# Kernel optimization log

Hardware: AMD Instinct MI355X
Metric: run time of the kernel (lower is better)

The kernel has to match this reference:

```python
import jax, jax.numpy as jnp
import numpy as np

NUM_EMBEDDINGS = 1024
EMBEDDING_DIM = 64
COMMITMENT_COST = 0.1
DECAY = 0.9
EPSILON = 1e-05


def setup_inputs() -> dict:
    key = jax.random.key(0)
    k1, k2, k3 = jax.random.split(key, 3)
    inputs = jax.random.normal(k1, (16, EMBEDDING_DIM, 4096), dtype=jnp.float32)
    embedding_weight = jax.random.normal(k2, (NUM_EMBEDDINGS, EMBEDDING_DIM), dtype=jnp.float32)
    ema_cluster_size = jnp.zeros((NUM_EMBEDDINGS,), dtype=jnp.float32)
    ema_w = jax.random.normal(k3, (NUM_EMBEDDINGS, EMBEDDING_DIM), dtype=jnp.float32)
    return {
        "inputs": inputs,
        "embedding_weight": embedding_weight,
        "ema_cluster_size": ema_cluster_size,
        "ema_w": ema_w,
    }


def reference(inputs, embedding_weight, ema_cluster_size, ema_w):
    K, D = embedding_weight.shape
    # (B, C, L) -> (B, L, C); C == embedding_dim
    x = jnp.transpose(inputs, (0, 2, 1))
    B, L, _ = x.shape
    flat = x.reshape(-1, D)  # [N, D], N = B*L
    N = flat.shape[0]

    distances = (
        jnp.sum(flat * flat, axis=1, keepdims=True)
        + jnp.sum(embedding_weight * embedding_weight, axis=1)
        - 2.0 * (flat @ embedding_weight.T)
    )
    idx = jnp.argmin(distances, axis=1)  # [N] int

    # embedding lookup (equivalent to one-hot @ weight)
    quantized = embedding_weight[idx].reshape(B, L, D)

    # one-hot column sums and scatter-reduction, without materializing [N, K]
    counts = jnp.zeros((K,), dtype=flat.dtype).at[idx].add(1.0)  # sum(encodings, 0)
    dw = jax.ops.segment_sum(flat, idx, num_segments=K)  # encodings^T @ flat_input

    # EMA updates (training path)
    cs = ema_cluster_size * DECAY + (1.0 - DECAY) * counts
    n = jnp.sum(cs)
    cs = (cs + EPSILON) / (n + K * EPSILON) * n
    new_ema_w = ema_w * DECAY + (1.0 - DECAY) * dw
    new_embedding_weight = new_ema_w / cs[:, None]

    # KLDivLoss(batchmean)(softmax(quantized.detach()), softmax(inputs)) over dim=2
    p_in = jax.nn.softmax(jax.lax.stop_gradient(quantized), axis=2)
    p_tgt = jax.nn.softmax(x, axis=2)
    kl = jnp.sum(p_tgt * (jnp.log(p_tgt) - p_in)) / B
    loss = COMMITMENT_COST * kl

    # straight-through estimator
    quantized_st = x + jax.lax.stop_gradient(quantized - x)

    avg_probs = counts / N
    perplexity = jnp.exp(-jnp.sum(avg_probs * jnp.log(avg_probs + 1e-10)))

    out = jnp.transpose(quantized_st, (0, 2, 1))  # back to (B, C, L)
    encoding_indices = idx[:, None]
    return (out, loss, perplexity, new_embedding_weight, encoding_indices)
```

## Files before the change

### kernel.cpp

```cpp
#include <hip/hip_runtime.h>

#define LDIM 4096
#define DDIM 64
#define KCODES 1024
#define BDIM 16
#define NROWS 65536
#define NSLICE 8
#define SLICE_ROWS (NROWS / NSLICE)

typedef __attribute__((ext_vector_type(8))) short short8;
typedef __attribute__((ext_vector_type(16))) float float16v;

__device__ __forceinline__ unsigned int orderf(float f) {
  unsigned int u = __float_as_uint(f);
  return (u & 0x80000000u) ? ~u : (u | 0x80000000u);
}

__device__ __forceinline__ unsigned long long shfl_xor_u64(unsigned long long v, int m) {
  int lo = __shfl_xor((int)(unsigned int)(v & 0xffffffffull), m, 64);
  int hi = __shfl_xor((int)(unsigned int)(v >> 32), m, 64);
  return ((unsigned long long)(unsigned int)hi << 32) | (unsigned int)lo;
}

__device__ __forceinline__ unsigned int bf16_rne(float x) {
  unsigned int u = __float_as_uint(x);
  return (u + 0x7FFFu + ((u >> 16) & 1u)) >> 16;
}

__global__ void prep_kernel(const float* __restrict__ Ew,
                            float* __restrict__ enorm,
                            float* __restrict__ SE,
                            unsigned short* __restrict__ Epk2) {
  int k = blockIdx.x;
  int d = threadIdx.x;
  float v = Ew[k * DDIM + d];
  float n2 = v * v;
  #pragma unroll
  for (int o = 32; o > 0; o >>= 1) n2 += __shfl_xor(n2, o, 64);
  float m = v;
  #pragma unroll
  for (int o = 32; o > 0; o >>= 1) m = fmaxf(m, __shfl_xor(m, o, 64));
  float e = __expf(v - m);
  float Z = e;
  #pragma unroll
  for (int o = 32; o > 0; o >>= 1) Z += __shfl_xor(Z, o, 64);
  SE[k * DDIM + d] = e / Z;
  if (d == 0) enorm[k] = n2;

  unsigned int rh = bf16_rne(v);
  float hif = __uint_as_float(rh << 16);
  unsigned int rl = bf16_rne(v - hif);
  int tile = k >> 5, mm = k & 31;
  int s = d >> 4, h = (d >> 3) & 1, j = d & 7;
  int base = tile * 4096 + (h * 32 + mm) * 8 + j;
  Epk2[base + s * 512]        = (unsigned short)rh;
  Epk2[base + (4 + s) * 512]  = (unsigned short)rl;
}

__launch_bounds__(256, 2)
__global__ void argmin_kernel(const float* __restrict__ inp,
                              const unsigned short* __restrict__ Epk2,
                              const float* __restrict__ enorm,
                              int* __restrict__ idx_ws,
                              float* __restrict__ outidx) {
  const int tid = threadIdx.x;
  const int lane = tid & 63;
  const int w = tid >> 6;
  const int half = lane >> 5;
  const int m = lane & 31;
  const int row_base = blockIdx.x * 128 + w * 32;
  const int b = row_base >> 12;
  const int l0 = row_base & 4095;
  const float* xp = inp + (size_t)b * DDIM * LDIM + l0 + m;

  short8 afr[8];
  #pragma unroll
  for (int s = 0; s < 4; s++) {
    #pragma unroll
    for (int j = 0; j < 8; j++) {
      int d = 16 * s + 8 * half + j;
      float x = xp[(size_t)d * LDIM];
      unsigned int rh = bf16_rne(x);
      float hif = __uint_as_float(rh << 16);
      unsigned int rl = bf16_rne(x - hif);
      afr[s][j] = (short)(unsigned short)rh;
      afr[4 + s][j] = (short)(unsigned short)rl;
    }
  }

  float bsc[16];
  int bix[16];
  #pragma unroll
  for (int j = 0; j < 16; j++) { bsc[j] = 1e30f; bix[j] = 0; }

  const unsigned short* eb = Epk2 + lane * 8;

  short8 bA[8], bB[8];
  float enA, enB;

  #pragma unroll
  for (int s = 0; s < 4; s++) {
    bA[s]     = *(const short8*)(eb + s * 512);
    bA[4 + s] = *(const short8*)(eb + 2048 + s * 512);
  }
  enA = enorm[m];

  #pragma unroll 1
  for (int i = 0; i < 16; i++) {
    const int tB = 2 * i + 1;
    {
      const unsigned short* p = eb + tB * 4096;
      #pragma unroll
      for (int s = 0; s < 4; s++) {
        bB[s]     = *(const short8*)(p + s * 512);
        bB[4 + s] = *(const short8*)(p + 2048 + s * 512);
      }
      enB = enorm[tB * 32 + m];
    }
    {
      float16v a0 = {}, a1 = {}, a2 = {};
      #pragma unroll
      for (int s = 0; s < 4; s++) {
        a0 = __builtin_amdgcn_mfma_f32_32x32x16_bf16(afr[s], bA[s], a0, 0, 0, 0);
        a1 = __builtin_amdgcn_mfma_f32_32x32x16_bf16(afr[s], bA[4 + s], a1, 0, 0, 0);
        a2 = __builtin_amdgcn_mfma_f32_32x32x16_bf16(afr[4 + s], bA[s], a2, 0, 0, 0);
      }
      int ci = 2 * i * 32 + m;
      #pragma unroll
      for (int j = 0; j < 16; j++) {
        float sc = fmaf(-2.f, a0[j] + a1[j] + a2[j], enA);
        if (sc < bsc[j]) { bsc[j] = sc; bix[j] = ci; }
      }
    }
    if (i < 15) {
      const unsigned short* p = eb + (2 * i + 2) * 4096;
      #pragma unroll
      for (int s = 0; s < 4; s++) {
        bA[s]     = *(const short8*)(p + s * 512);
        bA[4 + s] = *(const short8*)(p + 2048 + s * 512);
      }
      enA = enorm[(2 * i + 2) * 32 + m];
    }
    {
      float16v a0 = {}, a1 = {}, a2 = {};
      #pragma unroll
      for (int s = 0; s < 4; s++) {
        a0 = __builtin_amdgcn_mfma_f32_32x32x16_bf16(afr[s], bB[s], a0, 0, 0, 0);
        a1 = __builtin_amdgcn_mfma_f32_32x32x16_bf16(afr[s], bB[4 + s], a1, 0, 0, 0);
        a2 = __builtin_amdgcn_mfma_f32_32x32x16_bf16(afr[4 + s], bB[s], a2, 0, 0, 0);
      }
      int ci = tB * 32 + m;
      #pragma unroll
      for (int j = 0; j < 16; j++) {
        float sc = fmaf(-2.f, a0[j] + a1[j] + a2[j], enB);
        if (sc < bsc[j]) { bsc[j] = sc; bix[j] = ci; }
      }
    }
  }

  #pragma unroll
  for (int j = 0; j < 16; j++) {
    unsigned long long key =
        ((unsigned long long)orderf(bsc[j]) << 32) | (unsigned int)bix[j];
    #pragma unroll
    for (int mm = 1; mm < 32; mm <<= 1) {
      unsigned long long o = shfl_xor_u64(key, mm);
      if (o < key) key = o;
    }
    if (m == 0) {
      int row_local = (j & 3) + 8 * (j >> 2) + 4 * half;
      int grow = row_base + row_local;
      int cidx = (int)(key & 0xffffffffull);
      idx_ws[grow] = cidx;
      outidx[grow] = (float)cidx;
    }
  }
}

__launch_bounds__(256)
__global__ void outkl_dw_kernel(const float* __restrict__ inp,
                                const float* __restrict__ Ew,
                                const float* __restrict__ SE,
                                const int* __restrict__ idx_ws,
                                float* __restrict__ out,
                                float* __restrict__ klacc,
                                float* __restrict__ partial,
                                float* __restrict__ pcounts) {
  __shared__ float lds[2 * KCODES];
  const int tid = threadIdx.x;

  if (blockIdx.x < 1024) {
    float* Zs  = lds;
    float* S1s = lds + 256;
    float* Us  = lds + 512;
    const int c = tid >> 6;
    const int i = tid & 63;
    const int r = blockIdx.x * 64 + i;
    const int b = r >> 12, l = r & 4095;
    const float* xp = inp + (size_t)b * DDIM * LDIM + l;
    float* op = out + (size_t)b * DDIM * LDIM + l;
    const int k = idx_ws[r];
    const float4* Ek4 = (const float4*)(Ew + k * DDIM) + c * 4;
    const float4* Qk4 = (const float4*)(SE + k * DDIM) + c * 4;

    float Z = 0.f, S1 = 0.f, U = 0.f;
    #pragma unroll
    for (int t = 0; t < 4; t++) {
      float ek[4], qk[4];
      *(float4*)ek = Ek4[t];
      *(float4*)qk = Qk4[t];
      #pragma unroll
      for (int u = 0; u < 4; u++) {
        int d = c * 16 + t * 4 + u;
        float x = xp[(size_t)d * LDIM];
        float e = __expf(x);
        Z += e;
        S1 += e * x;
        U += e * qk[u];
        op[(size_t)d * LDIM] = ek[u];
      }
    }
    Zs[c * 64 + i] = Z; S1s[c * 64 + i] = S1; Us[c * 64 + i] = U;
    __syncthreads();
    if (tid < 64) {
      float Zt = Zs[i] + Zs[64 + i] + Zs[128 + i] + Zs[192 + i];
      float S1t = S1s[i] + S1s[64 + i] + S1s[128 + i] + S1s[192 + i];
      float Ut = Us[i] + Us[64 + i] + Us[128 + i] + Us[192 + i];
      float kl = (S1t - Ut) / Zt - __logf(Zt);
      #pragma unroll
      for (int o = 32; o > 0; o >>= 1) kl += __shfl_xor(kl, o, 64);
      if (i == 0) atomicAdd(klacc, kl);
    }
  } else {
    float* dwp = lds;
    float* cnt = lds + KCODES;
    const int bid = blockIdx.x - 1024;
    const int d = bid & 63;
    const int slice = bid >> 6;
    const bool do_cnt = (d == 0);

    #pragma unroll
    for (int i = 0; i < KCODES / 256; i++) {
      dwp[tid + i * 256] = 0.f;
      cnt[tid + i * 256] = 0.f;
    }
    __syncthreads();

    const int r0 = slice * SLICE_ROWS;
    for (int i = tid; i < SLICE_ROWS; i += 256) {
      int r = r0 + i;
      int b = r >> 12, l = r & 4095;
      float x = inp[(size_t)b * DDIM * LDIM + (size_t)d * LDIM + l];
      int k = idx_ws[r];
      atomicAdd(&dwp[k], x);
      if (do_cnt) atomicAdd(&cnt[k], 1.0f);
    }
    __syncthreads();

    float* dst = partial + ((size_t)slice * 64 + d) * KCODES;
    #pragma unroll
    for (int i = 0; i < KCODES / 256; i++) dst[tid + i * 256] = dwp[tid + i * 256];
    if (do_cnt) {
      float* cd = pcounts + (size_t)slice * KCODES;
      #pragma unroll
      for (int i = 0; i < KCODES / 256; i++) cd[tid + i * 256] = cnt[tid + i * 256];
    }
  }
}

__launch_bounds__(256)
__global__ void finalize_kernel(const float* __restrict__ partial,
                                const float* __restrict__ pcounts,
                                const float* __restrict__ emaw,
                                const float* __restrict__ emacs,
                                const float* __restrict__ klacc,
                                float* __restrict__ emb_out,
                                float* __restrict__ loss_out,
                                float* __restrict__ perp_out) {
  __shared__ float red[4], red2[4];
  const int tid = threadIdx.x;
  const int i = blockIdx.x * 256 + tid;
  const int k = i >> 6, d = i & 63;

  float se = 0.f;
  #pragma unroll
  for (int t = 0; t < 4; t++) se += emacs[tid * 4 + t];
  #pragma unroll
  for (int o = 32; o > 0; o >>= 1) se += __shfl_xor(se, o, 64);
  if ((tid & 63) == 0) red[tid >> 6] = se;
  __syncthreads();
  const float S = red[0] + red[1] + red[2] + red[3];
  const float N = 0.9f * S + 0.1f * (float)NROWS;

  float c = 0.f;
  #pragma unroll
  for (int sl = 0; sl < NSLICE; sl++) c += pcounts[sl * KCODES + k];
  float cs = fmaf(0.1f, c, emacs[k] * 0.9f);
  float csp = (cs + 1e-5f) / (N + (float)KCODES * 1e-5f) * N;

  float s = 0.f;
  #pragma unroll
  for (int sl = 0; sl < NSLICE; sl++)
    s += partial[((size_t)sl * 64 + d) * KCODES + k];
  emb_out[i] = fmaf(0.1f, s, emaw[i] * 0.9f) / csp;

  if (blockIdx.x == 0) {
    float es = 0.f;
    #pragma unroll
    for (int t = 0; t < 4; t++) {
      int kk = tid * 4 + t;
      float cc = 0.f;
      #pragma unroll
      for (int sl = 0; sl < NSLICE; sl++) cc += pcounts[sl * KCODES + kk];
      float a = cc * (1.0f / (float)NROWS);
      es += a * logf(a + 1e-10f);
    }
    #pragma unroll
    for (int o = 32; o > 0; o >>= 1) es += __shfl_xor(es, o, 64);
    if ((tid & 63) == 0) red2[tid >> 6] = es;
    __syncthreads();
    if (tid == 0) {
      *perp_out = expf(-(red2[0] + red2[1] + red2[2] + red2[3]));
      *loss_out = 0.1f * (*klacc) * (1.0f / 16.0f);
    }
  }
}

extern "C" void kernel_launch(void* const* d_in, const int* in_sizes, int n_in,
                              void* d_out, int out_size, void* d_ws, size_t ws_size,
                              hipStream_t stream) {
  const float* inp   = (const float*)d_in[0];
  const float* Ew    = (const float*)d_in[1];
  const float* emacs = (const float*)d_in[2];
  const float* emaw  = (const float*)d_in[3];

  float* out      = (float*)d_out;
  float* loss_out = out + 4194304;
  float* perp_out = out + 4194305;
  float* emb_out  = out + 4194306;
  float* idxf_out = out + 4194306 + 65536;

  char* ws = (char*)d_ws;
  int*   idx_ws  = (int*)(ws);
  float* klacc   = (float*)(ws + 262144);
  float* enorm   = (float*)(ws + 266496);
  float* SE      = (float*)(ws + 274688);
  unsigned short* Epk2 = (unsigned short*)(ws + 536832);
  float* partial = (float*)(ws + 536832);
  float* pcounts = (float*)(ws + 2633984);

  hipMemsetAsync(ws + 262144, 0, 256, stream);

  prep_kernel<<<KCODES, 64, 0, stream>>>(Ew, enorm, SE, Epk2);
  argmin_kernel<<<512, 256, 0, stream>>>(inp, Epk2, enorm, idx_ws, idxf_out);
  outkl_dw_kernel<<<1536, 256, 0, stream>>>(inp, Ew, SE, idx_ws, out, klacc,
                                            partial, pcounts);
  finalize_kernel<<<NROWS / 256, 256, 0, stream>>>(partial, pcounts, emaw, emacs,
                                                   klacc, emb_out, loss_out,
                                                   perp_out);
}
```

Before: 164.1 us.

## Restage codeword gather through LDS for vectorized output writes and KL

The output/KL branch now handles 256 rows per block instead of 64. Each block gathers the selected codewords and softmax rows into LDS in transposed form, so input reads and output writes become float4 accesses along L rather than scalar strided accesses. Block order is swapped so the scatter-reduction (dw) blocks launch first, and the grid shrinks from 1536 to 768 blocks. The cost is about 46KB of LDS per block, which reduces occupancy, plus extra __syncthreads per 16-dim chunk.

```diff
diff --git a/kernel.cpp b/kernel.cpp
--- a/kernel.cpp
+++ b/kernel.cpp
@@ -186,57 +186,14 @@
                                 float* __restrict__ klacc,
                                 float* __restrict__ partial,
                                 float* __restrict__ pcounts) {
-  __shared__ float lds[2 * KCODES];
+  __shared__ float smem[11528];
   const int tid = threadIdx.x;
 
-  if (blockIdx.x < 1024) {
-    float* Zs  = lds;
-    float* S1s = lds + 256;
-    float* Us  = lds + 512;
-    const int c = tid >> 6;
-    const int i = tid & 63;
-    const int r = blockIdx.x * 64 + i;
-    const int b = r >> 12, l = r & 4095;
-    const float* xp = inp + (size_t)b * DDIM * LDIM + l;
-    float* op = out + (size_t)b * DDIM * LDIM + l;
-    const int k = idx_ws[r];
-    const float4* Ek4 = (const float4*)(Ew + k * DDIM) + c * 4;
-    const float4* Qk4 = (const float4*)(SE + k * DDIM) + c * 4;
-
-    float Z = 0.f, S1 = 0.f, U = 0.f;
-    #pragma unroll
-    for (int t = 0; t < 4; t++) {
-      float ek[4], qk[4];
-      *(float4*)ek = Ek4[t];
-      *(float4*)qk = Qk4[t];
-      #pragma unroll
-      for (int u = 0; u < 4; u++) {
-        int d = c * 16 + t * 4 + u;
-        float x = xp[(size_t)d * LDIM];
-        float e = __expf(x);
-        Z += e;
-        S1 += e * x;
-        U += e * qk[u];
-        op[(size_t)d * LDIM] = ek[u];
-      }
-    }
-    Zs[c * 64 + i] = Z; S1s[c * 64 + i] = S1; Us[c * 64 + i] = U;
-    __syncthreads();
-    if (tid < 64) {
-      float Zt = Zs[i] + Zs[64 + i] + Zs[128 + i] + Zs[192 + i];
-      float S1t = S1s[i] + S1s[64 + i] + S1s[128 + i] + S1s[192 + i];
-      float Ut = Us[i] + Us[64 + i] + Us[128 + i] + Us[192 + i];
-      float kl = (S1t - Ut) / Zt - __logf(Zt);
-      #pragma unroll
-      for (int o = 32; o > 0; o >>= 1) kl += __shfl_xor(kl, o, 64);
-      if (i == 0) atomicAdd(klacc, kl);
-    }
-  } else {
-    float* dwp = lds;
-    float* cnt = lds + KCODES;
-    const int bid = blockIdx.x - 1024;
-    const int d = bid & 63;
-    const int slice = bid >> 6;
+  if (blockIdx.x < 512) {
+    float* dwp = smem;
+    float* cnt = smem + KCODES;
+    const int d = blockIdx.x & 63;
+    const int slice = blockIdx.x >> 6;
     const bool do_cnt = (d == 0);
 
     #pragma unroll
@@ -265,6 +222,91 @@
       #pragma unroll
       for (int i = 0; i < KCODES / 256; i++) cd[tid + i * 256] = cnt[tid + i * 256];
     }
+  } else {
+    int*   kk  = (int*)smem;
+    float* Et  = smem + 256;
+    float* Qt  = smem + 4352;
+    float* Zp  = smem + 8448;
+    float* S1p = smem + 9472;
+    float* Up  = smem + 10496;
+    float* red4 = smem + 11520;
+
+    const int obid = blockIdx.x - 512;
+    const int r0 = obid * 256;
+    const int b = r0 >> 12;
+    const int l0 = r0 & 4095;
+    const float* xbase = inp + (size_t)b * DDIM * LDIM + l0;
+    float* obase = out + (size_t)b * DDIM * LDIM + l0;
+    const int w = tid >> 6, lane = tid & 63;
+
+    kk[tid] = idx_ws[r0 + tid];
+    __syncthreads();
+    const int myk = kk[tid];
+    const int gi = ((tid & 3) << 6) | (tid >> 2);
+
+    float Zc[4] = {0.f, 0.f, 0.f, 0.f};
+    float S1c[4] = {0.f, 0.f, 0.f, 0.f};
+    float Uc[4] = {0.f, 0.f, 0.f, 0.f};
+
+    #pragma unroll 1
+    for (int c = 0; c < 4; c++) {
+      {
+        const float4* Ep = (const float4*)(Ew + myk * DDIM + c * 16);
+        const float4* Qp = (const float4*)(SE + myk * DDIM + c * 16);
+        #pragma unroll
+        for (int q = 0; q < 4; q++) {
+          float4 ev = Ep[q], qv = Qp[q];
+          Et[(4 * q + 0) * 256 + tid] = ev.x;
+          Et[(4 * q + 1) * 256 + tid] = ev.y;
+          Et[(4 * q + 2) * 256 + tid] = ev.z;
+          Et[(4 * q + 3) * 256 + tid] = ev.w;
+          Qt[(4 * q + 0) * 256 + gi] = qv.x;
+          Qt[(4 * q + 1) * 256 + gi] = qv.y;
+          Qt[(4 * q + 2) * 256 + gi] = qv.z;
+          Qt[(4 * q + 3) * 256 + gi] = qv.w;
+        }
+      }
+      __syncthreads();
+      #pragma unroll
+      for (int t = 0; t < 4; t++) {
+        const int dq = 4 * w + t;
+        const int d = c * 16 + dq;
+        float4 xv = *(const float4*)(xbase + (size_t)d * LDIM + lane * 4);
+        float4 ov = *(const float4*)&Et[dq * 256 + lane * 4];
+        *(float4*)(obase + (size_t)d * LDIM + lane * 4) = ov;
+        #pragma unroll
+        for (int j = 0; j < 4; j++) {
+          float x = (j == 0) ? xv.x : (j == 1) ? xv.y : (j == 2) ? xv.z : xv.w;
+          float e = __expf(x);
+          Zc[j] += e;
+          S1c[j] += e * x;
+          Uc[j] += e * Qt[dq * 256 + (j << 6) + lane];
+        }
+      }
+      __syncthreads();
+    }
+
+    #pragma unroll
+    for (int j = 0; j < 4; j++) {
+      Zp[w * 256 + 4 * lane + j] = Zc[j];
+      S1p[w * 256 + 4 * lane + j] = S1c[j];
+      Up[w * 256 + 4 * lane + j] = Uc[j];
+    }
+    __syncthreads();
+    float Z = 0.f, S1 = 0.f, U = 0.f;
+    #pragma unroll
+    for (int w2 = 0; w2 < 4; w2++) {
+      Z += Zp[w2 * 256 + tid];
+      S1 += S1p[w2 * 256 + tid];
+      U += Up[w2 * 256 + tid];
+    }
+    float kl = (S1 - U) / Z - __logf(Z);
+    #pragma unroll
+    for (int o = 32; o > 0; o >>= 1) kl += __shfl_xor(kl, o, 64);
+    if (lane == 0) red4[w] = kl;
+    __syncthreads();
+    if (tid == 0)
+      atomicAdd(klacc, red4[0] + red4[1] + red4[2] + red4[3]);
   }
 }
 
@@ -353,8 +395,8 @@
 
   prep_kernel<<<KCODES, 64, 0, stream>>>(Ew, enorm, SE, Epk2);
   argmin_kernel<<<512, 256, 0, stream>>>(inp, Epk2, enorm, idx_ws, idxf_out);
-  outkl_dw_kernel<<<1536, 256, 0, stream>>>(inp, Ew, SE, idx_ws, out, klacc,
-                                            partial, pcounts);
+  outkl_dw_kernel<<<768, 256, 0, stream>>>(inp, Ew, SE, idx_ws, out, klacc,
+                                           partial, pcounts);
   finalize_kernel<<<NROWS / 256, 256, 0, stream>>>(partial, pcounts, emaw, emacs,
                                                    klacc, emb_out, loss_out,
                                                    perp_out);
```

Measured after the change: 162.7 us. About the same (-0.8%).
